# Optimization experiments

Measured on AMD Instinct MI355X. Metric: run time of the kernel, lower is better.

Reference implementation:

```python
import jax, jax.numpy as jnp
import numpy as np
import math

D, H, FF = 1024, 16, 4096
B, L = 4, 1024

def setup_inputs() -> dict:
    key = jax.random.key(0)
    ks = jax.random.split(key, 20)
    g = lambda k, shp: jax.random.normal(k, shp, dtype=jnp.float32) * 0.02
    inp = {
        'x': jax.random.normal(ks[0], (B, L, D), dtype=jnp.float32),
        'encoder_output': jax.random.normal(ks[1], (B, L, D), dtype=jnp.float32),
        'src_mask': jnp.ones((1, 1, L, L), dtype=jnp.int32),
        'tgt_mask': jnp.tril(jnp.ones((L, L), dtype=jnp.int32))[None, None],
        'wq': g(ks[2], (D, D)), 'bq': jnp.zeros((D,), jnp.float32),
        'wk': g(ks[3], (D, D)), 'bk': jnp.zeros((D,), jnp.float32),
        'wv': g(ks[4], (D, D)), 'bv': jnp.zeros((D,), jnp.float32),
        'wo': g(ks[5], (D, D)), 'bo': jnp.zeros((D,), jnp.float32),
        'w1': g(ks[6], (FF, D)), 'b1': jnp.zeros((FF,), jnp.float32),
        'w2': g(ks[7], (D, FF)), 'b2': jnp.zeros((D,), jnp.float32),
        'g1': jnp.ones((D,), jnp.float32), 'be1': jnp.zeros((D,), jnp.float32),
        'g2': jnp.ones((D,), jnp.float32), 'be2': jnp.zeros((D,), jnp.float32),
    }
    return inp

def _layernorm(x, g, b, eps=1e-5):
    mu = jnp.mean(x, axis=-1, keepdims=True)
    var = jnp.var(x, axis=-1, keepdims=True)
    return (x - mu) * jax.lax.rsqrt(var + eps) * g + b

def _mha(q, k, v, mask, wq, bq, wk, bk, wv, bv, wo, bo):
    Bq, Lq, C = q.shape
    dh = C // H
    qh = (q @ wq.T + bq).reshape(Bq, Lq, H, dh)      # b q h d
    kh = (k @ wk.T + bk).reshape(Bq, -1, H, dh)       # b k h d
    vh = (v @ wv.T + bv).reshape(Bq, -1, H, dh)
    # NOTE: source scales by sqrt(C) (full model dim), not sqrt(head_dim)
    scores = jnp.einsum('bqhd,bkhd->bhqk', qh, kh) / math.sqrt(C)
    if mask is not None:
        scores = jnp.where(mask == 0, jnp.float32(-1e9), scores)
    attn = jax.nn.softmax(scores, axis=-1)
    out = jnp.einsum('bhqk,bkhd->bqhd', attn, vh).reshape(Bq, Lq, C)
    return out @ wo.T + bo

def reference(x, encoder_output, src_mask, tgt_mask,
              wq, bq, wk, bk, wv, bv, wo, bo,
              w1, b1, w2, b2, g1, be1, g2, be2):
    # self-attention (dropout identity in eval mode)
    y1 = _mha(x, x, x, tgt_mask, wq, bq, wk, bk, wv, bv, wo, bo)
    y1 = _layernorm(y1 + x, g1, be1)
    # cross-attention: source reuses attn1 weights and layer_norm1 (faithful)
    y2 = _mha(y1, encoder_output, encoder_output, src_mask, wq, bq, wk, bk, wv, bv, wo, bo)
    y2 = _layernorm(y1 + y2, g1, be1)
    # FFN + layer_norm2
    y = jax.nn.relu(y2 @ w1.T + b1) @ w2.T + b2
    return _layernorm(y2 + y, g2, be2)
```

## Files before the change

### kernel.cpp

```cpp
#include <hip/hip_runtime.h>
#include <hip/hip_bf16.h>

typedef __attribute__((ext_vector_type(8))) short short8;
typedef __attribute__((ext_vector_type(4))) float f32x4;
typedef __attribute__((ext_vector_type(4))) unsigned short ushort4v;

#define MFMA_BF16(a, b, c) __builtin_amdgcn_mfma_f32_16x16x32_bf16((a), (b), (c), 0, 0, 0)
#define AS1 __attribute__((address_space(1)))
#define AS3 __attribute__((address_space(3)))

__device__ __forceinline__ unsigned short f2b(float f) {
  unsigned u = __float_as_uint(f);
  u += 0x7fffu + ((u >> 16) & 1u);
  return (unsigned short)(u >> 16);
}

__device__ __forceinline__ size_t kpack_idx(int row, int col) {
  int b = row >> 10, l = row & 1023, h = col >> 6, d = col & 63;
  return ((size_t)(b * 16 + h) << 16) + l * 64 + (d ^ ((l & 7) << 3));
}
__device__ __forceinline__ size_t vpack_idx(int row, int col) {
  int b = row >> 10, k = row & 1023, h = col >> 6, d = col & 63;
  int kt = k >> 6, kk = k & 63;
  return ((size_t)((b * 16 + h) * 16 + kt) << 12) + d * 64 + (kk ^ ((d & 7) << 3));
}

__global__ __launch_bounds__(256) void cast8(
    const float* s0, const float* s1, const float* s2, const float* s3,
    const float* s4, const float* s5, const float* s6, const float* s7,
    unsigned short* d0, unsigned short* d1, unsigned short* d2, unsigned short* d3,
    unsigned short* d4, unsigned short* d5, unsigned short* d6, unsigned short* d7,
    int n0, int n1, int n2, int n3, int n4, int n5, int n6, int n7) {
  const float* s; unsigned short* d; int n;
  switch (blockIdx.y) {
    case 0: s = s0; d = d0; n = n0; break;
    case 1: s = s1; d = d1; n = n1; break;
    case 2: s = s2; d = d2; n = n2; break;
    case 3: s = s3; d = d3; n = n3; break;
    case 4: s = s4; d = d4; n = n4; break;
    case 5: s = s5; d = d5; n = n5; break;
    case 6: s = s6; d = d6; n = n6; break;
    default: s = s7; d = d7; n = n7; break;
  }
  int stride = gridDim.x * blockDim.x;
  for (int i = blockIdx.x * blockDim.x + threadIdx.x; i < n; i += stride) {
    float4 v = reinterpret_cast<const float4*>(s)[i];
    ushort4v o;
    o.x = f2b(v.x); o.y = f2b(v.y); o.z = f2b(v.z); o.w = f2b(v.w);
    reinterpret_cast<ushort4v*>(d)[i] = o;
  }
}

template <int RELU, int RES, int OUTF, int OUTB, int TM>
__global__ __launch_bounds__(256) void gemm_bt(
    const unsigned short* __restrict__ A, const unsigned short* __restrict__ W,
    const float* __restrict__ bias, const float* __restrict__ resid,
    float* __restrict__ outF, unsigned short* __restrict__ outB,
    int M, int N, int K) {
  constexpr int MI = TM / 32;
  __shared__ unsigned short lA[TM * 32];
  __shared__ unsigned short lB[128 * 32];
  int nbn = N >> 7;
  int nwg = gridDim.x;
  int id = blockIdx.x;
  { int q = nwg >> 3; id = (id & 7) * q + (id >> 3); }
  int m0 = (id / nbn) * TM, n0 = (id % nbn) << 7;
  int lane = threadIdx.x & 63, wave = threadIdx.x >> 6;
  int wr = (wave >> 1) * (TM / 2), wc = (wave & 1) * 64;
  int rq = lane & 15, kq = (lane >> 4) * 8;
  f32x4 acc[MI][4] = {};

  int e0 = wave * 512 + lane * 8;
  for (int kt = 0; kt < K; kt += 32) {
#pragma unroll
    for (int i = 0; i < TM / 64; ++i) {
      int e = e0 + i * 2048;
      int row = e >> 5, col = e & 31;
      __builtin_amdgcn_global_load_lds(
          (const AS1 void*)(A + (size_t)(m0 + row) * K + kt + col),
          (AS3 void*)(lA + i * 2048 + wave * 512), 16, 0, 0);
    }
#pragma unroll
    for (int i = 0; i < 2; ++i) {
      int e = e0 + i * 2048;
      int row = e >> 5, col = e & 31;
      __builtin_amdgcn_global_load_lds(
          (const AS1 void*)(W + (size_t)(n0 + row) * K + kt + col),
          (AS3 void*)(lB + i * 2048 + wave * 512), 16, 0, 0);
    }
    __syncthreads();
    short8 af[MI], bf[4];
#pragma unroll
    for (int i = 0; i < MI; ++i)
      af[i] = *reinterpret_cast<const short8*>(lA + (wr + i * 16 + rq) * 32 + kq);
#pragma unroll
    for (int j = 0; j < 4; ++j)
      bf[j] = *reinterpret_cast<const short8*>(lB + (wc + j * 16 + rq) * 32 + kq);
#pragma unroll
    for (int i = 0; i < MI; ++i)
#pragma unroll
      for (int j = 0; j < 4; ++j)
        acc[i][j] = MFMA_BF16(af[i], bf[j], acc[i][j]);
    __syncthreads();
  }

  int r0 = (lane >> 4) * 4;
#pragma unroll
  for (int i = 0; i < MI; ++i) {
#pragma unroll
    for (int j = 0; j < 4; ++j) {
      int row = m0 + wr + i * 16 + r0;
      int col = n0 + wc + j * 16 + rq;
      float bv = bias[col];
#pragma unroll
      for (int r = 0; r < 4; ++r) {
        float v = acc[i][j][r] + bv;
        if (RES) v += resid[(size_t)(row + r) * N + col];
        if (RELU) v = fmaxf(v, 0.0f);
        if (OUTF) outF[(size_t)(row + r) * N + col] = v;
        if (OUTB) outB[(size_t)(row + r) * N + col] = f2b(v);
      }
    }
  }
}

__global__ __launch_bounds__(256) void gemm_qkv(
    const unsigned short* __restrict__ xb, const unsigned short* __restrict__ encb,
    const unsigned short* __restrict__ wq, const unsigned short* __restrict__ wk,
    const unsigned short* __restrict__ wv,
    const float* __restrict__ bq, const float* __restrict__ bk, const float* __restrict__ bv,
    unsigned short* __restrict__ qb, unsigned short* __restrict__ kp1,
    unsigned short* __restrict__ vp1, unsigned short* __restrict__ kp2,
    unsigned short* __restrict__ vp2) {
  __shared__ unsigned short lA[128 * 32];
  __shared__ unsigned short lB[128 * 32];
  int id = blockIdx.x;
  id = (id & 7) * 160 + (id >> 3);
  int im = id / 40, jn = id % 40;
  int sel = jn >> 3;
  int m0 = im << 7, col0 = (jn & 7) << 7;
  const unsigned short* A = (sel < 3) ? xb : encb;
  const unsigned short* Wm = (sel == 0) ? wq : ((sel == 1 || sel == 3) ? wk : wv);
  const float* bias = (sel == 0) ? bq : ((sel == 1 || sel == 3) ? bk : bv);
  int lane = threadIdx.x & 63, wave = threadIdx.x >> 6;
  int wr = (wave >> 1) * 64, wc = (wave & 1) * 64;
  int rq = lane & 15, kq = (lane >> 4) * 8;
  f32x4 acc[4][4] = {};

  int e0 = wave * 512 + lane * 8;
  for (int kt = 0; kt < 1024; kt += 32) {
#pragma unroll
    for (int i = 0; i < 2; ++i) {
      int e = e0 + i * 2048;
      int row = e >> 5, col = e & 31;
      __builtin_amdgcn_global_load_lds(
          (const AS1 void*)(A + (size_t)(m0 + row) * 1024 + kt + col),
          (AS3 void*)(lA + i * 2048 + wave * 512), 16, 0, 0);
      __builtin_amdgcn_global_load_lds(
          (const AS1 void*)(Wm + (size_t)(col0 + row) * 1024 + kt + col),
          (AS3 void*)(lB + i * 2048 + wave * 512), 16, 0, 0);
    }
    __syncthreads();
    short8 af[4], bf[4];
#pragma unroll
    for (int i = 0; i < 4; ++i)
      af[i] = *reinterpret_cast<const short8*>(lA + (wr + i * 16 + rq) * 32 + kq);
#pragma unroll
    for (int j = 0; j < 4; ++j)
      bf[j] = *reinterpret_cast<const short8*>(lB + (wc + j * 16 + rq) * 32 + kq);
#pragma unroll
    for (int i = 0; i < 4; ++i)
#pragma unroll
      for (int j = 0; j < 4; ++j)
        acc[i][j] = MFMA_BF16(af[i], bf[j], acc[i][j]);
    __syncthreads();
  }

  unsigned short* outp = (sel == 0) ? qb : (sel == 1) ? kp1 : (sel == 2) ? vp1
                         : (sel == 3) ? kp2 : vp2;
  int pack = (sel == 0) ? 0 : ((sel == 1 || sel == 3) ? 1 : 2);
  int r0 = (lane >> 4) * 4;
#pragma unroll
  for (int i = 0; i < 4; ++i) {
#pragma unroll
    for (int j = 0; j < 4; ++j) {
      int row0 = m0 + wr + i * 16 + r0;
      int col = col0 + wc + j * 16 + rq;
      float bv = bias[col];
#pragma unroll
      for (int r = 0; r < 4; ++r) {
        int row = row0 + r;
        float v = acc[i][j][r] + bv;
        if (pack == 0) outp[(size_t)row * 1024 + col] = f2b(v);
        else if (pack == 1) outp[kpack_idx(row, col)] = f2b(v);
        else outp[vpack_idx(row, col)] = f2b(v);
      }
    }
  }
}

__global__ __launch_bounds__(256) void attn_kernel(
    const unsigned short* __restrict__ Q, const unsigned short* __restrict__ Kp,
    const unsigned short* __restrict__ Vp, unsigned short* __restrict__ O, int causal) {
  __shared__ unsigned short kls[2][4096];
  __shared__ unsigned short vls[2][4096];
  __shared__ unsigned short pls[4][1024];
  int id = blockIdx.x;
  int xcd = id & 7, j = id >> 3;
  int bh = xcd * 8 + (j & 7);
  int b = bh >> 4, h = bh & 15;
  int lane = threadIdx.x & 63, wave = threadIdx.x >> 6;
  int rq = lane & 15, hi = lane >> 4, kq = hi * 8;
  int xr = (rq & 7) << 3;
  int sb = wave * 1024 + lane * 8;
  const float SC = 0.04508422f;

  const unsigned short* Kbh = Kp + ((size_t)bh << 16);
  const unsigned short* Vbh = Vp + ((size_t)bh << 16);

  int p = j >> 3;
  int nt = causal ? 2 : 1;
  for (int ti = 0; ti < nt; ++ti) {
    int qt = causal ? (ti == 0 ? p : 15 - p) : p;
    int qrow0 = qt * 64 + wave * 16;
    const unsigned short* Qb = Q + (size_t)(b * 1024 + qrow0) * 1024 + h * 64;
    short8 qf[2];
#pragma unroll
    for (int c = 0; c < 2; ++c)
      qf[c] = *reinterpret_cast<const short8*>(Qb + (size_t)rq * 1024 + c * 32 + kq);

    int nkt = causal ? (qt + 1) : 16;
#pragma unroll
    for (int i = 0; i < 2; ++i) {
      __builtin_amdgcn_global_load_lds((const AS1 void*)(Kbh + sb + i * 512),
                                       (AS3 void*)(&kls[0][sb + i * 512]), 16, 0, 0);
      __builtin_amdgcn_global_load_lds((const AS1 void*)(Vbh + sb + i * 512),
                                       (AS3 void*)(&vls[0][sb + i * 512]), 16, 0, 0);
    }
    __syncthreads();

    float m2 = -1e30f, lsum = 0.f;
    f32x4 accd[4] = {};
    int cur = 0;
    for (int kt = 0; kt < nkt; ++kt) {
      if (kt + 1 < nkt) {
        const unsigned short* kg = Kbh + (kt + 1) * 4096 + sb;
        const unsigned short* vg = Vbh + (kt + 1) * 4096 + sb;
#pragma unroll
        for (int i = 0; i < 2; ++i) {
          __builtin_amdgcn_global_load_lds((const AS1 void*)(kg + i * 512),
                                           (AS3 void*)(&kls[cur ^ 1][sb + i * 512]), 16, 0, 0);
          __builtin_amdgcn_global_load_lds((const AS1 void*)(vg + i * 512),
                                           (AS3 void*)(&vls[cur ^ 1][sb + i * 512]), 16, 0, 0);
        }
      }
      f32x4 st[4];
#pragma unroll
      for (int sub = 0; sub < 4; ++sub) {
        f32x4 z = {0.f, 0.f, 0.f, 0.f};
#pragma unroll
        for (int c = 0; c < 2; ++c) {
          short8 kf = *reinterpret_cast<const short8*>(
              &kls[cur][(sub * 16 + rq) * 64 + ((c * 32 + hi * 8) ^ xr)]);
          z = MFMA_BF16(kf, qf[c], z);
        }
        st[sub] = z * SC;
      }
      if (causal && kt == qt) {
#pragma unroll
        for (int sub = 0; sub < 4; ++sub)
#pragma unroll
          for (int r = 0; r < 4; ++r)
            if (sub * 16 + hi * 4 + r > wave * 16 + rq) st[sub][r] = -1e9f;
      }
      f32x4 t0 = {fmaxf(st[0][0], st[1][0]), fmaxf(st[0][1], st[1][1]),
                  fmaxf(st[0][2], st[1][2]), fmaxf(st[0][3], st[1][3])};
      f32x4 t1 = {fmaxf(st[2][0], st[3][0]), fmaxf(st[2][1], st[3][1]),
                  fmaxf(st[2][2], st[3][2]), fmaxf(st[2][3], st[3][3])};
      float mx = fmaxf(fmaxf(fmaxf(t0[0], t1[0]), fmaxf(t0[1], t1[1])),
                       fmaxf(fmaxf(t0[2], t1[2]), fmaxf(t0[3], t1[3])));
      mx = fmaxf(mx, __shfl_xor(mx, 16, 64));
      mx = fmaxf(mx, __shfl_xor(mx, 32, 64));
      float mn = fmaxf(m2, mx);
      float al = exp2f(m2 - mn);
      m2 = mn;
      f32x4 e[4];
#pragma unroll
      for (int sub = 0; sub < 4; ++sub)
#pragma unroll
        for (int r = 0; r < 4; ++r) e[sub][r] = exp2f(st[sub][r] - mn);
      f32x4 s01 = e[0] + e[1], s23 = e[2] + e[3];
      f32x4 s = s01 + s23;
      float ps = (s[0] + s[1]) + (s[2] + s[3]);
      ps += __shfl_xor(ps, 16, 64);
      ps += __shfl_xor(ps, 32, 64);
      lsum = lsum * al + ps;
#pragma unroll
      for (int sub = 0; sub < 4; ++sub) {
        unsigned w0 = (unsigned)f2b(e[sub][0]) | ((unsigned)f2b(e[sub][1]) << 16);
        unsigned w1 = (unsigned)f2b(e[sub][2]) | ((unsigned)f2b(e[sub][3]) << 16);
        uint2 w = make_uint2(w0, w1);
        *reinterpret_cast<uint2*>(&pls[wave][rq * 64 + ((sub * 16 + hi * 4) ^ xr)]) = w;
      }
      float alb[4];
#pragma unroll
      for (int r = 0; r < 4; ++r) alb[r] = __shfl(al, hi * 4 + r, 64);
#pragma unroll
      for (int d = 0; d < 4; ++d)
#pragma unroll
        for (int r = 0; r < 4; ++r) accd[d][r] *= alb[r];
      short8 pf[2];
#pragma unroll
      for (int c = 0; c < 2; ++c)
        pf[c] = *reinterpret_cast<const short8*>(&pls[wave][rq * 64 + ((c * 32 + hi * 8) ^ xr)]);
#pragma unroll
      for (int d = 0; d < 4; ++d) {
#pragma unroll
        for (int c = 0; c < 2; ++c) {
          short8 vf = *reinterpret_cast<const short8*>(
              &vls[cur][(d * 16 + rq) * 64 + ((c * 32 + hi * 8) ^ xr)]);
          accd[d] = MFMA_BF16(pf[c], vf, accd[d]);
        }
      }
      __syncthreads();
      cur ^= 1;
    }
    float lb[4];
#pragma unroll
    for (int r = 0; r < 4; ++r) lb[r] = 1.0f / __shfl(lsum, hi * 4 + r, 64);
#pragma unroll
    for (int d = 0; d < 4; ++d)
#pragma unroll
      for (int r = 0; r < 4; ++r)
        O[(size_t)(b * 1024 + qrow0 + hi * 4 + r) * 1024 + h * 64 + d * 16 + rq] =
            f2b(accd[d][r] * lb[r]);
  }
}

template <int OUTF, int OUTB>
__global__ __launch_bounds__(256) void ln_kernel(const float* __restrict__ X,
                                                 const float* __restrict__ g,
                                                 const float* __restrict__ be,
                                                 float* __restrict__ outF,
                                                 unsigned short* __restrict__ outB) {
  __shared__ float red[2][4];
  int row = blockIdx.x;
  int t = threadIdx.x;
  const float* xr = X + (size_t)row * 1024;
  float4 v = reinterpret_cast<const float4*>(xr)[t];
  float s = v.x + v.y + v.z + v.w;
  float ss = v.x * v.x + v.y * v.y + v.z * v.z + v.w * v.w;
#pragma unroll
  for (int off = 1; off < 64; off <<= 1) {
    s += __shfl_xor(s, off, 64);
    ss += __shfl_xor(ss, off, 64);
  }
  int wave = t >> 6;
  if ((t & 63) == 0) { red[0][wave] = s; red[1][wave] = ss; }
  __syncthreads();
  s = red[0][0] + red[0][1] + red[0][2] + red[0][3];
  ss = red[1][0] + red[1][1] + red[1][2] + red[1][3];
  float mu = s * (1.f / 1024.f);
  float var = ss * (1.f / 1024.f) - mu * mu;
  float rs = rsqrtf(var + 1e-5f);
  float4 gv = reinterpret_cast<const float4*>(g)[t];
  float4 bv = reinterpret_cast<const float4*>(be)[t];
  float o0 = (v.x - mu) * rs * gv.x + bv.x;
  float o1 = (v.y - mu) * rs * gv.y + bv.y;
  float o2 = (v.z - mu) * rs * gv.z + bv.z;
  float o3 = (v.w - mu) * rs * gv.w + bv.w;
  if (OUTF) {
    float4 o = make_float4(o0, o1, o2, o3);
    reinterpret_cast<float4*>(outF + (size_t)row * 1024)[t] = o;
  }
  if (OUTB) {
    ushort4v o;
    o.x = f2b(o0); o.y = f2b(o1); o.z = f2b(o2); o.w = f2b(o3);
    reinterpret_cast<ushort4v*>(outB + (size_t)row * 1024)[t] = o;
  }
}

extern "C" void kernel_launch(void* const* d_in, const int* in_sizes, int n_in,
                              void* d_out, int out_size, void* d_ws, size_t ws_size,
                              hipStream_t stream) {
  const float* x   = (const float*)d_in[0];
  const float* enc = (const float*)d_in[1];
  const float* wq = (const float*)d_in[4];  const float* bq = (const float*)d_in[5];
  const float* wk = (const float*)d_in[6];  const float* bk = (const float*)d_in[7];
  const float* wv = (const float*)d_in[8];  const float* bv = (const float*)d_in[9];
  const float* wo = (const float*)d_in[10]; const float* bo = (const float*)d_in[11];
  const float* w1 = (const float*)d_in[12]; const float* b1 = (const float*)d_in[13];
  const float* w2 = (const float*)d_in[14]; const float* b2 = (const float*)d_in[15];
  const float* g1 = (const float*)d_in[16]; const float* be1 = (const float*)d_in[17];
  const float* g2 = (const float*)d_in[18]; const float* be2 = (const float*)d_in[19];
  float* out = (float*)d_out;

  const int M = 4096;
  char* ws = (char*)d_ws;
  size_t off = 0;
  auto alloc = [&](size_t bytes) -> char* {
    char* p = ws + off;
    off += (bytes + 255) & ~(size_t)255;
    return p;
  };
  unsigned short* xb   = (unsigned short*)alloc((size_t)M * 1024 * 2);
  unsigned short* encb = (unsigned short*)alloc((size_t)M * 1024 * 2);
  unsigned short* wqb  = (unsigned short*)alloc((size_t)1024 * 1024 * 2);
  unsigned short* wkb  = (unsigned short*)alloc((size_t)1024 * 1024 * 2);
  unsigned short* wvb  = (unsigned short*)alloc((size_t)1024 * 1024 * 2);
  unsigned short* wob  = (unsigned short*)alloc((size_t)1024 * 1024 * 2);
  unsigned short* w1b  = (unsigned short*)alloc((size_t)4096 * 1024 * 2);
  unsigned short* w2b  = (unsigned short*)alloc((size_t)4096 * 1024 * 2);
  unsigned short* qb   = (unsigned short*)alloc((size_t)M * 1024 * 2);
  unsigned short* kp1  = (unsigned short*)alloc((size_t)M * 1024 * 2);
  unsigned short* vp1  = (unsigned short*)alloc((size_t)M * 1024 * 2);
  unsigned short* kp2  = (unsigned short*)alloc((size_t)M * 1024 * 2);
  unsigned short* vp2  = (unsigned short*)alloc((size_t)M * 1024 * 2);
  unsigned short* ab   = (unsigned short*)alloc((size_t)M * 1024 * 2);
  float* s1 = (float*)alloc((size_t)M * 1024 * 4);
  float* y1 = (float*)alloc((size_t)M * 1024 * 4);
  unsigned short* hb = kp1;
  unsigned short* y1b = xb;
  unsigned short* y2b = qb;
  float* y2 = y1;

  dim3 b256(256);
  cast8<<<dim3(256, 8), b256, 0, stream>>>(
      x, enc, wq, wk, wv, wo, w1, w2,
      xb, encb, wqb, wkb, wvb, wob, w1b, w2b,
      M * 1024 / 4, M * 1024 / 4, 262144, 262144, 262144, 262144,
      4096 * 1024 / 4, 4096 * 1024 / 4);

  gemm_qkv<<<1280, b256, 0, stream>>>(xb, encb, wqb, wkb, wvb, bq, bk, bv,
                                      qb, kp1, vp1, kp2, vp2);

  attn_kernel<<<512, b256, 0, stream>>>(qb, kp1, vp1, ab, 1);
  gemm_bt<0, 1, 1, 0, 64><<<512, b256, 0, stream>>>(ab, wob, bo, x, s1, nullptr, M, 1024, 1024);
  ln_kernel<1, 1><<<4096, b256, 0, stream>>>(s1, g1, be1, y1, y1b);

  gemm_bt<0, 0, 0, 1, 64><<<512, b256, 0, stream>>>(y1b, wqb, bq, nullptr, nullptr, qb, M, 1024, 1024);
  attn_kernel<<<1024, b256, 0, stream>>>(qb, kp2, vp2, ab, 0);
  gemm_bt<0, 1, 1, 0, 64><<<512, b256, 0, stream>>>(ab, wob, bo, y1, s1, nullptr, M, 1024, 1024);
  ln_kernel<1, 1><<<4096, b256, 0, stream>>>(s1, g1, be1, y2, y2b);

  gemm_bt<1, 0, 0, 1, 128><<<1024, b256, 0, stream>>>(y2b, w1b, b1, nullptr, nullptr, hb, M, 4096, 1024);
  gemm_bt<0, 1, 1, 0, 64><<<512, b256, 0, stream>>>(hb, w2b, b2, y2, s1, nullptr, M, 1024, 4096);
  ln_kernel<1, 0><<<4096, b256, 0, stream>>>(s1, g2, be2, out, nullptr);

  (void)in_sizes; (void)n_in; (void)out_size; (void)ws_size;
}
```

Before: 385.1 us.

## Share K/V tiles across two query tiles in attention and deepen GEMM K-step

The attention kernel now processes two query tiles per block in one pass over the K/V tiles, so each loaded tile feeds both. Causal mode interleaves a short and a long query range, and non-causal mode pairs tiles p and p+8 with half the grid. The GEMMs switch to a 64-wide K step with XOR-swizzled LDS to halve barrier count, and the V-packed epilogue writes 4 bf16 values as one vector store. This raises LDS use and register pressure and halves attention block count, which may reduce occupancy.

After: 354.9 us. -7.8%, faster.

```diff
diff --git a/kernel.cpp b/kernel.cpp
--- a/kernel.cpp
+++ b/kernel.cpp
@@ -18,11 +18,6 @@
 __device__ __forceinline__ size_t kpack_idx(int row, int col) {
   int b = row >> 10, l = row & 1023, h = col >> 6, d = col & 63;
   return ((size_t)(b * 16 + h) << 16) + l * 64 + (d ^ ((l & 7) << 3));
-}
-__device__ __forceinline__ size_t vpack_idx(int row, int col) {
-  int b = row >> 10, k = row & 1023, h = col >> 6, d = col & 63;
-  int kt = k >> 6, kk = k & 63;
-  return ((size_t)((b * 16 + h) * 16 + kt) << 12) + d * 64 + (kk ^ ((d & 7) << 3));
 }
 
 __global__ __launch_bounds__(256) void cast8(
@@ -58,8 +53,8 @@
     float* __restrict__ outF, unsigned short* __restrict__ outB,
     int M, int N, int K) {
   constexpr int MI = TM / 32;
-  __shared__ unsigned short lA[TM * 32];
-  __shared__ unsigned short lB[128 * 32];
+  __shared__ unsigned short lA[TM * 64];
+  __shared__ unsigned short lB[128 * 64];
   int nbn = N >> 7;
   int nwg = gridDim.x;
   int id = blockIdx.x;
@@ -68,39 +63,45 @@
   int lane = threadIdx.x & 63, wave = threadIdx.x >> 6;
   int wr = (wave >> 1) * (TM / 2), wc = (wave & 1) * 64;
   int rq = lane & 15, kq = (lane >> 4) * 8;
+  int xr8 = (rq & 7) << 3;
   f32x4 acc[MI][4] = {};
 
-  int e0 = wave * 512 + lane * 8;
-  for (int kt = 0; kt < K; kt += 32) {
-#pragma unroll
-    for (int i = 0; i < TM / 64; ++i) {
-      int e = e0 + i * 2048;
-      int row = e >> 5, col = e & 31;
+  int t8 = threadIdx.x * 8;
+  for (int kt = 0; kt < K; kt += 64) {
+#pragma unroll
+    for (int i = 0; i < MI; ++i) {
+      int e = t8 + i * 2048;
+      int row = e >> 6;
+      int gcol = (((e >> 3) & 7) ^ (row & 7)) << 3;
       __builtin_amdgcn_global_load_lds(
-          (const AS1 void*)(A + (size_t)(m0 + row) * K + kt + col),
-          (AS3 void*)(lA + i * 2048 + wave * 512), 16, 0, 0);
-    }
-#pragma unroll
-    for (int i = 0; i < 2; ++i) {
-      int e = e0 + i * 2048;
-      int row = e >> 5, col = e & 31;
+          (const AS1 void*)(A + (size_t)(m0 + row) * K + kt + gcol),
+          (AS3 void*)(lA + e), 16, 0, 0);
+    }
+#pragma unroll
+    for (int i = 0; i < 4; ++i) {
+      int e = t8 + i * 2048;
+      int row = e >> 6;
+      int gcol = (((e >> 3) & 7) ^ (row & 7)) << 3;
       __builtin_amdgcn_global_load_lds(
-          (const AS1 void*)(W + (size_t)(n0 + row) * K + kt + col),
-          (AS3 void*)(lB + i * 2048 + wave * 512), 16, 0, 0);
+          (const AS1 void*)(W + (size_t)(n0 + row) * K + kt + gcol),
+          (AS3 void*)(lB + e), 16, 0, 0);
     }
     __syncthreads();
-    short8 af[MI], bf[4];
-#pragma unroll
-    for (int i = 0; i < MI; ++i)
-      af[i] = *reinterpret_cast<const short8*>(lA + (wr + i * 16 + rq) * 32 + kq);
-#pragma unroll
-    for (int j = 0; j < 4; ++j)
-      bf[j] = *reinterpret_cast<const short8*>(lB + (wc + j * 16 + rq) * 32 + kq);
-#pragma unroll
-    for (int i = 0; i < MI; ++i)
+#pragma unroll
+    for (int s = 0; s < 2; ++s) {
+      short8 af[MI], bf[4];
+#pragma unroll
+      for (int i = 0; i < MI; ++i)
+        af[i] = *reinterpret_cast<const short8*>(lA + (wr + i * 16 + rq) * 64 + ((s * 32 + kq) ^ xr8));
 #pragma unroll
       for (int j = 0; j < 4; ++j)
-        acc[i][j] = MFMA_BF16(af[i], bf[j], acc[i][j]);
+        bf[j] = *reinterpret_cast<const short8*>(lB + (wc + j * 16 + rq) * 64 + ((s * 32 + kq) ^ xr8));
+#pragma unroll
+      for (int i = 0; i < MI; ++i)
+#pragma unroll
+        for (int j = 0; j < 4; ++j)
+          acc[i][j] = MFMA_BF16(af[i], bf[j], acc[i][j]);
+    }
     __syncthreads();
   }
 
@@ -132,8 +133,8 @@
     unsigned short* __restrict__ qb, unsigned short* __restrict__ kp1,
     unsigned short* __restrict__ vp1, unsigned short* __restrict__ kp2,
     unsigned short* __restrict__ vp2) {
-  __shared__ unsigned short lA[128 * 32];
-  __shared__ unsigned short lB[128 * 32];
+  __shared__ unsigned short lA[128 * 64];
+  __shared__ unsigned short lB[128 * 64];
   int id = blockIdx.x;
   id = (id & 7) * 160 + (id >> 3);
   int im = id / 40, jn = id % 40;
@@ -145,34 +146,39 @@
   int lane = threadIdx.x & 63, wave = threadIdx.x >> 6;
   int wr = (wave >> 1) * 64, wc = (wave & 1) * 64;
   int rq = lane & 15, kq = (lane >> 4) * 8;
+  int xr8 = (rq & 7) << 3;
   f32x4 acc[4][4] = {};
 
-  int e0 = wave * 512 + lane * 8;
-  for (int kt = 0; kt < 1024; kt += 32) {
-#pragma unroll
-    for (int i = 0; i < 2; ++i) {
-      int e = e0 + i * 2048;
-      int row = e >> 5, col = e & 31;
+  int t8 = threadIdx.x * 8;
+  for (int kt = 0; kt < 1024; kt += 64) {
+#pragma unroll
+    for (int i = 0; i < 4; ++i) {
+      int e = t8 + i * 2048;
+      int row = e >> 6;
+      int gcol = (((e >> 3) & 7) ^ (row & 7)) << 3;
       __builtin_amdgcn_global_load_lds(
-          (const AS1 void*)(A + (size_t)(m0 + row) * 1024 + kt + col),
-          (AS3 void*)(lA + i * 2048 + wave * 512), 16, 0, 0);
+          (const AS1 void*)(A + (size_t)(m0 + row) * 1024 + kt + gcol),
+          (AS3 void*)(lA + e), 16, 0, 0);
       __builtin_amdgcn_global_load_lds(
-          (const AS1 void*)(Wm + (size_t)(col0 + row) * 1024 + kt + col),
-          (AS3 void*)(lB + i * 2048 + wave * 512), 16, 0, 0);
+          (const AS1 void*)(Wm + (size_t)(col0 + row) * 1024 + kt + gcol),
+          (AS3 void*)(lB + e), 16, 0, 0);
     }
     __syncthreads();
-    short8 af[4], bf[4];
-#pragma unroll
-    for (int i = 0; i < 4; ++i)
-      af[i] = *reinterpret_cast<const short8*>(lA + (wr + i * 16 + rq) * 32 + kq);
-#pragma unroll
-    for (int j = 0; j < 4; ++j)
-      bf[j] = *reinterpret_cast<const short8*>(lB + (wc + j * 16 + rq) * 32 + kq);
-#pragma unroll
-    for (int i = 0; i < 4; ++i)
+#pragma unroll
+    for (int s = 0; s < 2; ++s) {
+      short8 af[4], bf[4];
+#pragma unroll
+      for (int i = 0; i < 4; ++i)
+        af[i] = *reinterpret_cast<const short8*>(lA + (wr + i * 16 + rq) * 64 + ((s * 32 + kq) ^ xr8));
 #pragma unroll
       for (int j = 0; j < 4; ++j)
-        acc[i][j] = MFMA_BF16(af[i], bf[j], acc[i][j]);
+        bf[j] = *reinterpret_cast<const short8*>(lB + (wc + j * 16 + rq) * 64 + ((s * 32 + kq) ^ xr8));
+#pragma unroll
+      for (int i = 0; i < 4; ++i)
+#pragma unroll
+        for (int j = 0; j < 4; ++j)
+          acc[i][j] = MFMA_BF16(af[i], bf[j], acc[i][j]);
+    }
     __syncthreads();
   }
 
@@ -187,14 +193,100 @@
       int row0 = m0 + wr + i * 16 + r0;
       int col = col0 + wc + j * 16 + rq;
       float bv = bias[col];
-#pragma unroll
-      for (int r = 0; r < 4; ++r) {
-        int row = row0 + r;
-        float v = acc[i][j][r] + bv;
-        if (pack == 0) outp[(size_t)row * 1024 + col] = f2b(v);
-        else if (pack == 1) outp[kpack_idx(row, col)] = f2b(v);
-        else outp[vpack_idx(row, col)] = f2b(v);
+      if (pack == 2) {
+        int b = row0 >> 10, k0 = row0 & 1023, h = col >> 6, d = col & 63;
+        size_t idx = ((size_t)((b * 16 + h) * 16 + (k0 >> 6)) << 12) + d * 64 + ((k0 & 63) ^ ((d & 7) << 3));
+        ushort4v o;
+        o.x = f2b(acc[i][j][0] + bv);
+        o.y = f2b(acc[i][j][1] + bv);
+        o.z = f2b(acc[i][j][2] + bv);
+        o.w = f2b(acc[i][j][3] + bv);
+        *reinterpret_cast<ushort4v*>(&outp[idx]) = o;
+      } else {
+#pragma unroll
+        for (int r = 0; r < 4; ++r) {
+          int row = row0 + r;
+          float v = acc[i][j][r] + bv;
+          if (pack == 0) outp[(size_t)row * 1024 + col] = f2b(v);
+          else outp[kpack_idx(row, col)] = f2b(v);
+        }
       }
+    }
+  }
+}
+
+__device__ __forceinline__ void attn_step(
+    const unsigned short* __restrict__ kcur, const unsigned short* __restrict__ vcur,
+    unsigned short* __restrict__ plw, const short8* qf,
+    f32x4* accd, float& m2, float& lsum,
+    int rq, int hi, int kq, int xr, int wave, bool domask) {
+  const float SC = 0.04508422f;
+  f32x4 st[4];
+#pragma unroll
+  for (int sub = 0; sub < 4; ++sub) {
+    f32x4 z = {0.f, 0.f, 0.f, 0.f};
+#pragma unroll
+    for (int c = 0; c < 2; ++c) {
+      short8 kf = *reinterpret_cast<const short8*>(
+          &kcur[(sub * 16 + rq) * 64 + ((c * 32 + hi * 8) ^ xr)]);
+      z = MFMA_BF16(kf, qf[c], z);
+    }
+    st[sub] = z * SC;
+  }
+  if (domask) {
+#pragma unroll
+    for (int sub = 0; sub < 4; ++sub)
+#pragma unroll
+      for (int r = 0; r < 4; ++r)
+        if (sub * 16 + hi * 4 + r > wave * 16 + rq) st[sub][r] = -1e9f;
+  }
+  f32x4 t0 = {fmaxf(st[0][0], st[1][0]), fmaxf(st[0][1], st[1][1]),
+              fmaxf(st[0][2], st[1][2]), fmaxf(st[0][3], st[1][3])};
+  f32x4 t1 = {fmaxf(st[2][0], st[3][0]), fmaxf(st[2][1], st[3][1]),
+              fmaxf(st[2][2], st[3][2]), fmaxf(st[2][3], st[3][3])};
+  float mx = fmaxf(fmaxf(fmaxf(t0[0], t1[0]), fmaxf(t0[1], t1[1])),
+                   fmaxf(fmaxf(t0[2], t1[2]), fmaxf(t0[3], t1[3])));
+  mx = fmaxf(mx, __shfl_xor(mx, 16, 64));
+  mx = fmaxf(mx, __shfl_xor(mx, 32, 64));
+  float mn = fmaxf(m2, mx);
+  float al = exp2f(m2 - mn);
+  m2 = mn;
+  f32x4 e[4];
+#pragma unroll
+  for (int sub = 0; sub < 4; ++sub)
+#pragma unroll
+    for (int r = 0; r < 4; ++r) e[sub][r] = exp2f(st[sub][r] - mn);
+  f32x4 s01 = e[0] + e[1], s23 = e[2] + e[3];
+  f32x4 s = s01 + s23;
+  float ps = (s[0] + s[1]) + (s[2] + s[3]);
+  ps += __shfl_xor(ps, 16, 64);
+  ps += __shfl_xor(ps, 32, 64);
+  lsum = lsum * al + ps;
+#pragma unroll
+  for (int sub = 0; sub < 4; ++sub) {
+    unsigned w0 = (unsigned)f2b(e[sub][0]) | ((unsigned)f2b(e[sub][1]) << 16);
+    unsigned w1 = (unsigned)f2b(e[sub][2]) | ((unsigned)f2b(e[sub][3]) << 16);
+    uint2 w = make_uint2(w0, w1);
+    *reinterpret_cast<uint2*>(&plw[rq * 64 + ((sub * 16 + hi * 4) ^ xr)]) = w;
+  }
+  float alb[4];
+#pragma unroll
+  for (int r = 0; r < 4; ++r) alb[r] = __shfl(al, hi * 4 + r, 64);
+#pragma unroll
+  for (int d = 0; d < 4; ++d)
+#pragma unroll
+    for (int r = 0; r < 4; ++r) accd[d][r] *= alb[r];
+  short8 pf[2];
+#pragma unroll
+  for (int c = 0; c < 2; ++c)
+    pf[c] = *reinterpret_cast<const short8*>(&plw[rq * 64 + ((c * 32 + hi * 8) ^ xr)]);
+#pragma unroll
+  for (int d = 0; d < 4; ++d) {
+#pragma unroll
+    for (int c = 0; c < 2; ++c) {
+      short8 vf = *reinterpret_cast<const short8*>(
+          &vcur[(d * 16 + rq) * 64 + ((c * 32 + hi * 8) ^ xr)]);
+      accd[d] = MFMA_BF16(pf[c], vf, accd[d]);
     }
   }
 }
@@ -213,128 +305,75 @@
   int rq = lane & 15, hi = lane >> 4, kq = hi * 8;
   int xr = (rq & 7) << 3;
   int sb = wave * 1024 + lane * 8;
-  const float SC = 0.04508422f;
-
   const unsigned short* Kbh = Kp + ((size_t)bh << 16);
   const unsigned short* Vbh = Vp + ((size_t)bh << 16);
+  unsigned short* plw = pls[wave];
 
   int p = j >> 3;
-  int nt = causal ? 2 : 1;
-  for (int ti = 0; ti < nt; ++ti) {
-    int qt = causal ? (ti == 0 ? p : 15 - p) : p;
-    int qrow0 = qt * 64 + wave * 16;
-    const unsigned short* Qb = Q + (size_t)(b * 1024 + qrow0) * 1024 + h * 64;
-    short8 qf[2];
-#pragma unroll
-    for (int c = 0; c < 2; ++c)
-      qf[c] = *reinterpret_cast<const short8*>(Qb + (size_t)rq * 1024 + c * 32 + kq);
-
-    int nkt = causal ? (qt + 1) : 16;
-#pragma unroll
-    for (int i = 0; i < 2; ++i) {
-      __builtin_amdgcn_global_load_lds((const AS1 void*)(Kbh + sb + i * 512),
-                                       (AS3 void*)(&kls[0][sb + i * 512]), 16, 0, 0);
-      __builtin_amdgcn_global_load_lds((const AS1 void*)(Vbh + sb + i * 512),
-                                       (AS3 void*)(&vls[0][sb + i * 512]), 16, 0, 0);
-    }
+  int qtA = p;
+  int qtB = causal ? (15 - p) : (p + 8);
+  int lastA = causal ? qtA : 15;
+  int nkt = causal ? (qtB + 1) : 16;
+
+  int qrowA = qtA * 64 + wave * 16, qrowB = qtB * 64 + wave * 16;
+  short8 qfA[2], qfB[2];
+#pragma unroll
+  for (int c = 0; c < 2; ++c) {
+    qfA[c] = *reinterpret_cast<const short8*>(
+        Q + (size_t)(b * 1024 + qrowA + rq) * 1024 + h * 64 + c * 32 + kq);
+    qfB[c] = *reinterpret_cast<const short8*>(
+        Q + (size_t)(b * 1024 + qrowB + rq) * 1024 + h * 64 + c * 32 + kq);
+  }
+
+  float mA = -1e30f, lsA = 0.f, mB = -1e30f, lsB = 0.f;
+  f32x4 accA[4] = {}, accB[4] = {};
+
+#pragma unroll
+  for (int i = 0; i < 2; ++i) {
+    __builtin_amdgcn_global_load_lds((const AS1 void*)(Kbh + sb + i * 512),
+                                     (AS3 void*)(&kls[0][sb + i * 512]), 16, 0, 0);
+    __builtin_amdgcn_global_load_lds((const AS1 void*)(Vbh + sb + i * 512),
+                                     (AS3 void*)(&vls[0][sb + i * 512]), 16, 0, 0);
+  }
+  __syncthreads();
+
+  int cur = 0;
+  for (int kt = 0; kt < nkt; ++kt) {
+    if (kt + 1 < nkt) {
+      const unsigned short* kg = Kbh + (kt + 1) * 4096 + sb;
+      const unsigned short* vg = Vbh + (kt + 1) * 4096 + sb;
+#pragma unroll
+      for (int i = 0; i < 2; ++i) {
+        __builtin_amdgcn_global_load_lds((const AS1 void*)(kg + i * 512),
+                                         (AS3 void*)(&kls[cur ^ 1][sb + i * 512]), 16, 0, 0);
+        __builtin_amdgcn_global_load_lds((const AS1 void*)(vg + i * 512),
+                                         (AS3 void*)(&vls[cur ^ 1][sb + i * 512]), 16, 0, 0);
+      }
+    }
+    attn_step(kls[cur], vls[cur], plw, qfB, accB, mB, lsB, rq, hi, kq, xr, wave,
+              causal && kt == qtB);
+    if (kt <= lastA)
+      attn_step(kls[cur], vls[cur], plw, qfA, accA, mA, lsA, rq, hi, kq, xr, wave,
+                causal && kt == qtA);
     __syncthreads();
-
-    float m2 = -1e30f, lsum = 0.f;
-    f32x4 accd[4] = {};
-    int cur = 0;
-    for (int kt = 0; kt < nkt; ++kt) {
-      if (kt + 1 < nkt) {
-        const unsigned short* kg = Kbh + (kt + 1) * 4096 + sb;
-        const unsigned short* vg = Vbh + (kt + 1) * 4096 + sb;
-#pragma unroll
-        for (int i = 0; i < 2; ++i) {
-          __builtin_amdgcn_global_load_lds((const AS1 void*)(kg + i * 512),
-                                           (AS3 void*)(&kls[cur ^ 1][sb + i * 512]), 16, 0, 0);
-          __builtin_amdgcn_global_load_lds((const AS1 void*)(vg + i * 512),
-                                           (AS3 void*)(&vls[cur ^ 1][sb + i * 512]), 16, 0, 0);
-        }
-      }
-      f32x4 st[4];
-#pragma unroll
-      for (int sub = 0; sub < 4; ++sub) {
-        f32x4 z = {0.f, 0.f, 0.f, 0.f};
-#pragma unroll
-        for (int c = 0; c < 2; ++c) {
-          short8 kf = *reinterpret_cast<const short8*>(
-              &kls[cur][(sub * 16 + rq) * 64 + ((c * 32 + hi * 8) ^ xr)]);
-          z = MFMA_BF16(kf, qf[c], z);
-        }
-        st[sub] = z * SC;
-      }
-      if (causal && kt == qt) {
-#pragma unroll
-        for (int sub = 0; sub < 4; ++sub)
-#pragma unroll
-          for (int r = 0; r < 4; ++r)
-            if (sub * 16 + hi * 4 + r > wave * 16 + rq) st[sub][r] = -1e9f;
-      }
-      f32x4 t0 = {fmaxf(st[0][0], st[1][0]), fmaxf(st[0][1], st[1][1]),
-                  fmaxf(st[0][2], st[1][2]), fmaxf(st[0][3], st[1][3])};
-      f32x4 t1 = {fmaxf(st[2][0], st[3][0]), fmaxf(st[2][1], st[3][1]),
-                  fmaxf(st[2][2], st[3][2]), fmaxf(st[2][3], st[3][3])};
-      float mx = fmaxf(fmaxf(fmaxf(t0[0], t1[0]), fmaxf(t0[1], t1[1])),
-                       fmaxf(fmaxf(t0[2], t1[2]), fmaxf(t0[3], t1[3])));
-      mx = fmaxf(mx, __shfl_xor(mx, 16, 64));
-      mx = fmaxf(mx, __shfl_xor(mx, 32, 64));
-      float mn = fmaxf(m2, mx);
-      float al = exp2f(m2 - mn);
-      m2 = mn;
-      f32x4 e[4];
-#pragma unroll
-      for (int sub = 0; sub < 4; ++sub)
-#pragma unroll
-        for (int r = 0; r < 4; ++r) e[sub][r] = exp2f(st[sub][r] - mn);
-      f32x4 s01 = e[0] + e[1], s23 = e[2] + e[3];
-      f32x4 s = s01 + s23;
-      float ps = (s[0] + s[1]) + (s[2] + s[3]);
-      ps += __shfl_xor(ps, 16, 64);
-      ps += __shfl_xor(ps, 32, 64);
-      lsum = lsum * al + ps;
-#pragma unroll
-      for (int sub = 0; sub < 4; ++sub) {
-        unsigned w0 = (unsigned)f2b(e[sub][0]) | ((unsigned)f2b(e[sub][1]) << 16);
-        unsigned w1 = (unsigned)f2b(e[sub][2]) | ((unsigned)f2b(e[sub][3]) << 16);
-        uint2 w = make_uint2(w0, w1);
-        *reinterpret_cast<uint2*>(&pls[wave][rq * 64 + ((sub * 16 + hi * 4) ^ xr)]) = w;
-      }
-      float alb[4];
-#pragma unroll
-      for (int r = 0; r < 4; ++r) alb[r] = __shfl(al, hi * 4 + r, 64);
-#pragma unroll
-      for (int d = 0; d < 4; ++d)
-#pragma unroll
-        for (int r = 0; r < 4; ++r) accd[d][r] *= alb[r];
-      short8 pf[2];
-#pragma unroll
-      for (int c = 0; c < 2; ++c)
-        pf[c] = *reinterpret_cast<const short8*>(&pls[wave][rq * 64 + ((c * 32 + hi * 8) ^ xr)]);
-#pragma unroll
-      for (int d = 0; d < 4; ++d) {
-#pragma unroll
-        for (int c = 0; c < 2; ++c) {
-          short8 vf = *reinterpret_cast<const short8*>(
-              &vls[cur][(d * 16 + rq) * 64 + ((c * 32 + hi * 8) ^ xr)]);
-          accd[d] = MFMA_BF16(pf[c], vf, accd[d]);
-        }
-      }
-      __syncthreads();
-      cur ^= 1;
-    }
-    float lb[4];
-#pragma unroll
-    for (int r = 0; r < 4; ++r) lb[r] = 1.0f / __shfl(lsum, hi * 4 + r, 64);
-#pragma unroll
-    for (int d = 0; d < 4; ++d)
-#pragma unroll
-      for (int r = 0; r < 4; ++r)
-        O[(size_t)(b * 1024 + qrow0 + hi * 4 + r) * 1024 + h * 64 + d * 16 + rq] =
-            f2b(accd[d][r] * lb[r]);
-  }
+    cur ^= 1;
+  }
+
+  float lbA[4], lbB[4];
+#pragma unroll
+  for (int r = 0; r < 4; ++r) {
+    lbA[r] = 1.0f / __shfl(lsA, hi * 4 + r, 64);
+    lbB[r] = 1.0f / __shfl(lsB, hi * 4 + r, 64);
+  }
+#pragma unroll
+  for (int d = 0; d < 4; ++d)
+#pragma unroll
+    for (int r = 0; r < 4; ++r) {
+      O[(size_t)(b * 1024 + qrowA + hi * 4 + r) * 1024 + h * 64 + d * 16 + rq] =
+          f2b(accA[d][r] * lbA[r]);
+      O[(size_t)(b * 1024 + qrowB + hi * 4 + r) * 1024 + h * 64 + d * 16 + rq] =
+          f2b(accB[d][r] * lbB[r]);
+    }
 }
 
 template <int OUTF, int OUTB>
@@ -439,7 +478,7 @@
   ln_kernel<1, 1><<<4096, b256, 0, stream>>>(s1, g1, be1, y1, y1b);
 
   gemm_bt<0, 0, 0, 1, 64><<<512, b256, 0, stream>>>(y1b, wqb, bq, nullptr, nullptr, qb, M, 1024, 1024);
-  attn_kernel<<<1024, b256, 0, stream>>>(qb, kp2, vp2, ab, 0);
+  attn_kernel<<<512, b256, 0, stream>>>(qb, kp2, vp2, ab, 0);
   gemm_bt<0, 1, 1, 0, 64><<<512, b256, 0, stream>>>(ab, wob, bo, y1, s1, nullptr, M, 1024, 1024);
   ln_kernel<1, 1><<<4096, b256, 0, stream>>>(s1, g1, be1, y2, y2b);
 
```
